# Optimization experiments

Hardware: AMD Instinct MI355X
Metric: run time of the kernel (lower is better)

The kernel has to match this reference:

```python
import jax, jax.numpy as jnp
import numpy as np
from jax import lax


def setup_inputs() -> dict:
    key = jax.random.key(0)
    k1, k2 = jax.random.split(key)
    X = jax.random.normal(k1, (32, 64, 112, 112), dtype=jnp.float32)
    # module draws K ~ N(0, 0.01) each forward; we materialize it as a param
    K = 0.01 * jax.random.normal(k2, (128, 64, 3, 3), dtype=jnp.float32)
    return {"X": X, "K": K}


def reference(X, K):
    # Valid-padding cross-correlation, NCHW input, OIHW kernel, no bias.
    # Matches conv2d_multi_out: sum over in_channels, stack over out_channels.
    return lax.conv_general_dilated(
        X, K,
        window_strides=(1, 1),
        padding="VALID",
        dimension_numbers=("NCHW", "OIHW", "NCHW"),
    )
```

## Files before the change

kernel.cpp:

```cpp
#include <hip/hip_runtime.h>


typedef __attribute__((ext_vector_type(8)))  _Float16 f16x8;
typedef __attribute__((ext_vector_type(16))) float    f32x16;

struct __attribute__((aligned(4))) f2u { float x, y; };

constexpr int C_IN = 64, H = 112, W = 112;
constexpr int COUT = 128, OH = 110, OW = 110;
constexpr int NIMG = 32;
constexpr int KTOT = C_IN * 9;
constexpr int OSP  = OH * OW;
constexpr int SPTOT = NIMG * OSP;
constexpr int IMG_STRIDE = C_IN * H * W;
constexpr int CH_STRIDE  = H * W;
constexpr int LDC = 72;

__device__ __forceinline__ uint pkrtz_u32(float lo, float hi) {
    union { __fp16 __attribute__((ext_vector_type(2))) h; uint u; } c;
    c.h = __builtin_amdgcn_cvt_pkrtz(lo, hi);
    return c.u;
}

__device__ __forceinline__ int swz(int row, int chw) {
    return row * LDC + (chw ^ (((row >> 1) & 7) << 3));
}

__global__ void prep_a(const float* __restrict__ Kw, _Float16* __restrict__ A16) {
    int idx = blockIdx.x * 256 + threadIdx.x;
    if (idx >= COUT * KTOT) return;
    int cout = idx / KTOT, k = idx - cout * KTOT;
    int c = k / 9, s = k - c * 9;
    int o = c >> 3, j = c & 7;
    A16[((size_t)(s * 8 + o) * COUT + cout) * 8 + j] = (_Float16)Kw[idx];
}

__global__ __launch_bounds__(512, 4)
void conv_shift_f16(const float* __restrict__ X,
                    const _Float16* __restrict__ A16,
                    float* __restrict__ Out)
{
    __shared__ __align__(16) _Float16 Bs[2][128 * LDC];

    const int t = threadIdx.x;

    const int nwg = gridDim.x;
    const int q8 = nwg >> 3, r8 = nwg & 7;
    const int xcd = blockIdx.x & 7, idx8 = blockIdx.x >> 3;
    const int bid = (xcd < r8 ? xcd * (q8 + 1) : r8 * (q8 + 1) + (xcd - r8) * q8) + idx8;
    const int spBase = bid * 128;

    const int spp = t & 63;
    const int c0  = (t >> 6) << 3;
    const int sp0 = spBase + 2 * spp;
    const int nimg = sp0 / OSP;
    const int rsp  = sp0 - nimg * OSP;
    const int oh   = rsp / OW;
    const int ow   = rsp - oh * OW;
    const float* Xr = X + ((size_t)nimg * IMG_STRIDE + (size_t)c0 * CH_STRIDE + oh * W + ow);
    const int whw0 = swz(2 * spp,     c0);
    const int whw1 = swz(2 * spp + 1, c0);

    const int lane  = t & 63;
    const int wv    = t >> 6;
    const int wq    = wv >> 1;
    const int wc    = wv & 1;
    const int frow  = lane & 31;
    const int khalf = lane >> 5;
    const size_t arow = (size_t)(wq * 32 + frow) * 8;
    const int bmask = ((frow >> 1) & 7) << 3;
    const int brw0  = (wc * 64 + frow) * LDC;
    const int brw1  = (wc * 64 + 32 + frow) * LDC;

    f32x16 acc[2];
#pragma unroll
    for (int j = 0; j < 2; j++)
#pragma unroll
        for (int e = 0; e < 16; e++) acc[j][e] = 0.f;

    f2u g[8];

#define SOFF(S) (((S) / 3) * W + ((S) % 3))

#define GATHER(S)                                                              \
    {                                                                          \
        _Pragma("unroll")                                                      \
        for (int j = 0; j < 8; j++)                                            \
            g[j] = *reinterpret_cast<const f2u*>(Xr + (size_t)j * CH_STRIDE + SOFF(S)); \
    }

#define CVTWRITE(BUF)                                                          \
    {                                                                          \
        union { uint u[4]; f16x8 v; } px, py;                                  \
        _Pragma("unroll")                                                      \
        for (int p = 0; p < 4; p++) {                                          \
            px.u[p] = pkrtz_u32(g[2 * p].x, g[2 * p + 1].x);                   \
            py.u[p] = pkrtz_u32(g[2 * p].y, g[2 * p + 1].y);                   \
        }                                                                      \
        *reinterpret_cast<f16x8*>(&Bs[BUF][whw0]) = px.v;                      \
        *reinterpret_cast<f16x8*>(&Bs[BUF][whw1]) = py.v;                      \
    }

#define MFMA_STEP(S, B)                                                        \
    {                                                                          \
        _Pragma("unroll")                                                      \
        for (int kk = 0; kk < 4; kk++) {                                       \
            const size_t abase = (size_t)((S) * 8 + kk * 2 + khalf) * (COUT * 8) + arow; \
            const int chw = (kk * 16 + khalf * 8) ^ bmask;                     \
            f16x8 a0 = *reinterpret_cast<const f16x8*>(&A16[abase]);           \
            f16x8 b0 = *reinterpret_cast<const f16x8*>(&Bs[B][brw0 + chw]);    \
            f16x8 b1 = *reinterpret_cast<const f16x8*>(&Bs[B][brw1 + chw]);    \
            acc[0] = __builtin_amdgcn_mfma_f32_32x32x16_f16(a0, b0, acc[0], 0, 0, 0); \
            acc[1] = __builtin_amdgcn_mfma_f32_32x32x16_f16(a0, b1, acc[1], 0, 0, 0); \
        }                                                                      \
    }

    GATHER(0);
    CVTWRITE(0);
    GATHER(1);
    __syncthreads();

#pragma unroll
    for (int s = 0; s < 9; s++) {
        if (s < 8) CVTWRITE((s + 1) & 1);
        if (s < 7) GATHER(s + 2);
        MFMA_STEP(s, s & 1);
        __syncthreads();
    }

#undef GATHER
#undef CVTWRITE
#undef MFMA_STEP
#undef SOFF

#pragma unroll
    for (int j = 0; j < 2; j++) {
        const int sp2 = spBase + wc * 64 + j * 32 + frow;
        const int n2  = sp2 / OSP;
        const int r2  = sp2 - n2 * OSP;
        float* Ob = Out + (size_t)n2 * (COUT * OSP) + r2;
        const int cbase = wq * 32 + 4 * khalf;
#pragma unroll
        for (int reg = 0; reg < 16; reg++) {
            const int crow = cbase + (reg & 3) + 8 * (reg >> 2);
            Ob[(size_t)crow * OSP] = acc[j][reg];
        }
    }
}

extern "C" void kernel_launch(void* const* d_in, const int* in_sizes, int n_in,
                              void* d_out, int out_size, void* d_ws, size_t ws_size,
                              hipStream_t stream) {
    const float* X  = (const float*)d_in[0];
    const float* Kw = (const float*)d_in[1];
    float* Out = (float*)d_out;
    _Float16* A16 = (_Float16*)d_ws;

    prep_a<<<(COUT * KTOT + 255) / 256, 256, 0, stream>>>(Kw, A16);
    conv_shift_f16<<<SPTOT / 128, 512, 0, stream>>>(X, A16, Out);
}
```

Measured before the change: 111.6 us.

## Stage input rows in LDS once and reuse across all nine filter taps

Each workgroup now handles two output rows of one image. It loads the four input rows it needs, for all 64 channels, into shared memory as fp16 with a channel-slot swizzle. All 3x3 taps then read shifted windows of that staged tile instead of re-gathering X from global memory for every tap. This removes the 9x redundant global gather and the per-tap double buffering and barriers. In exchange, LDS use is larger (about 57KB), which may limit occupancy. About 220 of 256 spatial columns are used, so some MFMA work is wasted on padding.

Result: slower. 123.2 us (+10.5%).

```diff
diff --git a/kernel.cpp b/kernel.cpp
--- a/kernel.cpp
+++ b/kernel.cpp
@@ -4,26 +4,21 @@
 typedef __attribute__((ext_vector_type(8)))  _Float16 f16x8;
 typedef __attribute__((ext_vector_type(16))) float    f32x16;
 
-struct __attribute__((aligned(4))) f2u { float x, y; };
-
 constexpr int C_IN = 64, H = 112, W = 112;
 constexpr int COUT = 128, OH = 110, OW = 110;
 constexpr int NIMG = 32;
 constexpr int KTOT = C_IN * 9;
 constexpr int OSP  = OH * OW;
-constexpr int SPTOT = NIMG * OSP;
 constexpr int IMG_STRIDE = C_IN * H * W;
 constexpr int CH_STRIDE  = H * W;
-constexpr int LDC = 72;
+constexpr int ROWS = 4;
+constexpr int NRP  = OH / 2;
+constexpr int NWG  = NIMG * NRP;
 
 __device__ __forceinline__ uint pkrtz_u32(float lo, float hi) {
     union { __fp16 __attribute__((ext_vector_type(2))) h; uint u; } c;
     c.h = __builtin_amdgcn_cvt_pkrtz(lo, hi);
     return c.u;
-}
-
-__device__ __forceinline__ int swz(int row, int chw) {
-    return row * LDC + (chw ^ (((row >> 1) & 7) << 3));
 }
 
 __global__ void prep_a(const float* __restrict__ Kw, _Float16* __restrict__ A16) {
@@ -36,114 +31,105 @@
 }
 
 __global__ __launch_bounds__(512, 4)
-void conv_shift_f16(const float* __restrict__ X,
-                    const _Float16* __restrict__ A16,
-                    float* __restrict__ Out)
+void conv_resx_f16(const float* __restrict__ X,
+                   const _Float16* __restrict__ A16,
+                   float* __restrict__ Out)
 {
-    __shared__ __align__(16) _Float16 Bs[2][128 * LDC];
+    __shared__ __align__(16) _Float16 Xs[ROWS * W * C_IN];
 
     const int t = threadIdx.x;
 
-    const int nwg = gridDim.x;
-    const int q8 = nwg >> 3, r8 = nwg & 7;
-    const int xcd = blockIdx.x & 7, idx8 = blockIdx.x >> 3;
-    const int bid = (xcd < r8 ? xcd * (q8 + 1) : r8 * (q8 + 1) + (xcd - r8) * q8) + idx8;
-    const int spBase = bid * 128;
+    const int bid = (blockIdx.x & 7) * (NWG >> 3) + (blockIdx.x >> 3);
+    const int n   = bid / NRP;
+    const int rp  = bid - n * NRP;
+    const int oh0 = rp * 2;
 
-    const int spp = t & 63;
-    const int c0  = (t >> 6) << 3;
-    const int sp0 = spBase + 2 * spp;
-    const int nimg = sp0 / OSP;
-    const int rsp  = sp0 - nimg * OSP;
-    const int oh   = rsp / OW;
-    const int ow   = rsp - oh * OW;
-    const float* Xr = X + ((size_t)nimg * IMG_STRIDE + (size_t)c0 * CH_STRIDE + oh * W + ow);
-    const int whw0 = swz(2 * spp,     c0);
-    const int whw1 = swz(2 * spp + 1, c0);
+    const float* Xn = X + (size_t)n * IMG_STRIDE + (size_t)oh0 * W;
+
+    if (t < 448) {
+#pragma unroll
+        for (int q = 0; q < 4; q++) {
+            const int tau = q * 448 + t;
+            const int cg  = tau / 224;
+            const int wpr = tau - cg * 224;
+            const int row = wpr / 56;
+            const int wcl = (wpr - row * 56) * 2;
+            const float* src = Xn + (size_t)(cg * 8) * CH_STRIDE + row * W + wcl;
+            float2 v[8];
+#pragma unroll
+            for (int j = 0; j < 8; j++)
+                v[j] = *reinterpret_cast<const float2*>(src + (size_t)j * CH_STRIDE);
+            union { uint u[4]; f16x8 h; } p0, p1;
+#pragma unroll
+            for (int p = 0; p < 4; p++) {
+                p0.u[p] = pkrtz_u32(v[2 * p].x, v[2 * p + 1].x);
+                p1.u[p] = pkrtz_u32(v[2 * p].y, v[2 * p + 1].y);
+            }
+            const int a0 = (row * W + wcl)     * C_IN + ((cg ^ (wcl & 7)) << 3);
+            const int a1 = (row * W + wcl + 1) * C_IN + ((cg ^ ((wcl + 1) & 7)) << 3);
+            *reinterpret_cast<f16x8*>(&Xs[a0]) = p0.h;
+            *reinterpret_cast<f16x8*>(&Xs[a1]) = p1.h;
+        }
+    }
 
     const int lane  = t & 63;
     const int wv    = t >> 6;
-    const int wq    = wv >> 1;
-    const int wc    = wv & 1;
+    const int cq    = wv & 3;
+    const int sh    = wv >> 2;
     const int frow  = lane & 31;
     const int khalf = lane >> 5;
-    const size_t arow = (size_t)(wq * 32 + frow) * 8;
-    const int bmask = ((frow >> 1) & 7) << 3;
-    const int brw0  = (wc * 64 + frow) * LDC;
-    const int brw1  = (wc * 64 + 32 + frow) * LDC;
 
-    f32x16 acc[2];
+    int bbase[4], owv[4];
 #pragma unroll
-    for (int j = 0; j < 2; j++)
-#pragma unroll
-        for (int e = 0; e < 16; e++) acc[j][e] = 0.f;
-
-    f2u g[8];
-
-#define SOFF(S) (((S) / 3) * W + ((S) % 3))
-
-#define GATHER(S)                                                              \
-    {                                                                          \
-        _Pragma("unroll")                                                      \
-        for (int j = 0; j < 8; j++)                                            \
-            g[j] = *reinterpret_cast<const f2u*>(Xr + (size_t)j * CH_STRIDE + SOFF(S)); \
+    for (int i = 0; i < 4; i++) {
+        int spl = (sh * 4 + i) * 32 + frow;
+        int s2  = (spl < 220) ? spl : 0;
+        int orow = (s2 >= 110) ? 1 : 0;
+        int ow   = s2 - orow * 110;
+        bbase[i] = (orow * W + ow) * C_IN;
+        owv[i]   = ow;
     }
 
-#define CVTWRITE(BUF)                                                          \
-    {                                                                          \
-        union { uint u[4]; f16x8 v; } px, py;                                  \
-        _Pragma("unroll")                                                      \
-        for (int p = 0; p < 4; p++) {                                          \
-            px.u[p] = pkrtz_u32(g[2 * p].x, g[2 * p + 1].x);                   \
-            py.u[p] = pkrtz_u32(g[2 * p].y, g[2 * p + 1].y);                   \
-        }                                                                      \
-        *reinterpret_cast<f16x8*>(&Bs[BUF][whw0]) = px.v;                      \
-        *reinterpret_cast<f16x8*>(&Bs[BUF][whw1]) = py.v;                      \
-    }
+    f32x16 acc[4];
+#pragma unroll
+    for (int i = 0; i < 4; i++)
+#pragma unroll
+        for (int e = 0; e < 16; e++) acc[i][e] = 0.f;
 
-#define MFMA_STEP(S, B)                                                        \
-    {                                                                          \
-        _Pragma("unroll")                                                      \
-        for (int kk = 0; kk < 4; kk++) {                                       \
-            const size_t abase = (size_t)((S) * 8 + kk * 2 + khalf) * (COUT * 8) + arow; \
-            const int chw = (kk * 16 + khalf * 8) ^ bmask;                     \
-            f16x8 a0 = *reinterpret_cast<const f16x8*>(&A16[abase]);           \
-            f16x8 b0 = *reinterpret_cast<const f16x8*>(&Bs[B][brw0 + chw]);    \
-            f16x8 b1 = *reinterpret_cast<const f16x8*>(&Bs[B][brw1 + chw]);    \
-            acc[0] = __builtin_amdgcn_mfma_f32_32x32x16_f16(a0, b0, acc[0], 0, 0, 0); \
-            acc[1] = __builtin_amdgcn_mfma_f32_32x32x16_f16(a0, b1, acc[1], 0, 0, 0); \
-        }                                                                      \
-    }
-
-    GATHER(0);
-    CVTWRITE(0);
-    GATHER(1);
     __syncthreads();
 
 #pragma unroll
     for (int s = 0; s < 9; s++) {
-        if (s < 8) CVTWRITE((s + 1) & 1);
-        if (s < 7) GATHER(s + 2);
-        MFMA_STEP(s, s & 1);
-        __syncthreads();
+        const int kh = s / 3, kw = s % 3;
+        const int soff = (kh * W + kw) * C_IN;
+#pragma unroll
+        for (int kk = 0; kk < 4; kk++) {
+            const int oct = kk * 2;
+            const f16x8 a = *reinterpret_cast<const f16x8*>(
+                &A16[((size_t)((s * 8 + oct + khalf) * COUT) + cq * 32 + frow) * 8]);
+#pragma unroll
+            for (int i = 0; i < 4; i++) {
+                const int slot = ((oct + khalf) ^ ((owv[i] + kw) & 7)) << 3;
+                const f16x8 b = *reinterpret_cast<const f16x8*>(
+                    &Xs[bbase[i] + soff + slot]);
+                acc[i] = __builtin_amdgcn_mfma_f32_32x32x16_f16(a, b, acc[i], 0, 0, 0);
+            }
+        }
     }
 
-#undef GATHER
-#undef CVTWRITE
-#undef MFMA_STEP
-#undef SOFF
-
+    float* On = Out + (size_t)n * (COUT * (size_t)OSP) + (size_t)(cq * 32 + 4 * khalf) * OSP;
 #pragma unroll
-    for (int j = 0; j < 2; j++) {
-        const int sp2 = spBase + wc * 64 + j * 32 + frow;
-        const int n2  = sp2 / OSP;
-        const int r2  = sp2 - n2 * OSP;
-        float* Ob = Out + (size_t)n2 * (COUT * OSP) + r2;
-        const int cbase = wq * 32 + 4 * khalf;
+    for (int i = 0; i < 4; i++) {
+        const int spl = (sh * 4 + i) * 32 + frow;
+        if (spl < 220) {
+            const int orow = (spl >= 110) ? 1 : 0;
+            const int ow   = spl - orow * 110;
+            float* Ob = On + (size_t)(oh0 + orow) * OW + ow;
 #pragma unroll
-        for (int reg = 0; reg < 16; reg++) {
-            const int crow = cbase + (reg & 3) + 8 * (reg >> 2);
-            Ob[(size_t)crow * OSP] = acc[j][reg];
+            for (int reg = 0; reg < 16; reg++) {
+                const int crow = (reg & 3) + 8 * (reg >> 2);
+                Ob[(size_t)crow * OSP] = acc[i][reg];
+            }
         }
     }
 }
@@ -157,5 +143,5 @@
     _Float16* A16 = (_Float16*)d_ws;
 
     prep_a<<<(COUT * KTOT + 255) / 256, 256, 0, stream>>>(Kw, A16);
-    conv_shift_f16<<<SPTOT / 128, 512, 0, stream>>>(X, A16, Out);
+    conv_resx_f16<<<NWG, 512, 0, stream>>>(X, A16, Out);
 }
```

## Halve block size, stage weights in LDS via async loads, widen per-wave tile

Applied to the files above, without the earlier changes.

Moves from 512 to 256 threads per block, with each wave now computing 32 output channels across all 128 spatial positions (four accumulators instead of two). Weight slices for each filter tap are copied into a double-buffered LDS area with global_load_lds, so each A fragment is loaded once per step and reused across four MFMAs. Each thread now gathers 16 input channels per tap instead of 8, and the LDS swizzle is rewritten to match. This trades more registers and LDS per block, plus lower occupancy, for fewer global weight reads and more MFMA work per LDS read.

Result: slower. 141.8 us (+27.0%).

```diff
diff --git a/kernel.cpp b/kernel.cpp
--- a/kernel.cpp
+++ b/kernel.cpp
@@ -15,6 +15,7 @@
 constexpr int IMG_STRIDE = C_IN * H * W;
 constexpr int CH_STRIDE  = H * W;
 constexpr int LDC = 72;
+constexpr int ASLICE = 8 * COUT * 8;
 
 __device__ __forceinline__ uint pkrtz_u32(float lo, float hi) {
     union { __fp16 __attribute__((ext_vector_type(2))) h; uint u; } c;
@@ -22,9 +23,8 @@
     return c.u;
 }
 
-__device__ __forceinline__ int swz(int row, int chw) {
-    return row * LDC + (chw ^ (((row >> 1) & 7) << 3));
-}
+typedef __attribute__((address_space(3))) uint       lds_u32;
+typedef __attribute__((address_space(1))) const uint glb_u32;
 
 __global__ void prep_a(const float* __restrict__ Kw, _Float16* __restrict__ A16) {
     int idx = blockIdx.x * 256 + threadIdx.x;
@@ -35,12 +35,13 @@
     A16[((size_t)(s * 8 + o) * COUT + cout) * 8 + j] = (_Float16)Kw[idx];
 }
 
-__global__ __launch_bounds__(512, 4)
-void conv_shift_f16(const float* __restrict__ X,
-                    const _Float16* __restrict__ A16,
-                    float* __restrict__ Out)
+__global__ __launch_bounds__(256, 2)
+void conv_v6(const float* __restrict__ X,
+             const _Float16* __restrict__ A16,
+             float* __restrict__ Out)
 {
     __shared__ __align__(16) _Float16 Bs[2][128 * LDC];
+    __shared__ __align__(16) _Float16 As[2][ASLICE];
 
     const int t = threadIdx.x;
 
@@ -51,95 +52,115 @@
     const int spBase = bid * 128;
 
     const int spp = t & 63;
-    const int c0  = (t >> 6) << 3;
+    const int chh = t >> 6;
     const int sp0 = spBase + 2 * spp;
     const int nimg = sp0 / OSP;
     const int rsp  = sp0 - nimg * OSP;
     const int oh   = rsp / OW;
     const int ow   = rsp - oh * OW;
-    const float* Xr = X + ((size_t)nimg * IMG_STRIDE + (size_t)c0 * CH_STRIDE + oh * W + ow);
-    const int whw0 = swz(2 * spp,     c0);
-    const int whw1 = swz(2 * spp + 1, c0);
+    const float* Xb = X + ((size_t)nimg * IMG_STRIDE + (size_t)(chh * 16) * CH_STRIDE + oh * W + ow);
+    const int gsw = spp & 7;
+    const int wr0 = (2 * spp) * LDC;
+    const int wr1 = (2 * spp + 1) * LDC;
 
     const int lane  = t & 63;
-    const int wv    = t >> 6;
-    const int wq    = wv >> 1;
-    const int wc    = wv & 1;
+    const int cq    = t >> 6;
     const int frow  = lane & 31;
     const int khalf = lane >> 5;
-    const size_t arow = (size_t)(wq * 32 + frow) * 8;
-    const int bmask = ((frow >> 1) & 7) << 3;
-    const int brw0  = (wc * 64 + frow) * LDC;
-    const int brw1  = (wc * 64 + 32 + frow) * LDC;
+    const int bsw   = ((frow >> 1) & 7);
 
-    f32x16 acc[2];
+    f32x16 acc[4];
 #pragma unroll
-    for (int j = 0; j < 2; j++)
+    for (int j = 0; j < 4; j++)
 #pragma unroll
         for (int e = 0; e < 16; e++) acc[j][e] = 0.f;
 
-    f2u g[8];
+    f2u g[16];
 
 #define SOFF(S) (((S) / 3) * W + ((S) % 3))
 
 #define GATHER(S)                                                              \
     {                                                                          \
         _Pragma("unroll")                                                      \
-        for (int j = 0; j < 8; j++)                                            \
-            g[j] = *reinterpret_cast<const f2u*>(Xr + (size_t)j * CH_STRIDE + SOFF(S)); \
+        for (int c = 0; c < 16; c++)                                           \
+            g[c] = *reinterpret_cast<const f2u*>(Xb + (size_t)c * CH_STRIDE + SOFF(S)); \
     }
 
-#define CVTWRITE(BUF)                                                          \
+#define CVTWRITE(B)                                                            \
     {                                                                          \
-        union { uint u[4]; f16x8 v; } px, py;                                  \
         _Pragma("unroll")                                                      \
-        for (int p = 0; p < 4; p++) {                                          \
-            px.u[p] = pkrtz_u32(g[2 * p].x, g[2 * p + 1].x);                   \
-            py.u[p] = pkrtz_u32(g[2 * p].y, g[2 * p + 1].y);                   \
+        for (int o = 0; o < 2; o++) {                                          \
+            union { uint u[4]; f16x8 v; } px, py;                              \
+            _Pragma("unroll")                                                  \
+            for (int p = 0; p < 4; p++) {                                      \
+                px.u[p] = pkrtz_u32(g[o * 8 + 2 * p].x, g[o * 8 + 2 * p + 1].x); \
+                py.u[p] = pkrtz_u32(g[o * 8 + 2 * p].y, g[o * 8 + 2 * p + 1].y); \
+            }                                                                  \
+            const int slot = ((chh * 2 + o) ^ gsw) << 3;                       \
+            *reinterpret_cast<f16x8*>(&Bs[B][wr0 + slot]) = px.v;              \
+            *reinterpret_cast<f16x8*>(&Bs[B][wr1 + slot]) = py.v;              \
         }                                                                      \
-        *reinterpret_cast<f16x8*>(&Bs[BUF][whw0]) = px.v;                      \
-        *reinterpret_cast<f16x8*>(&Bs[BUF][whw1]) = py.v;                      \
     }
 
-#define MFMA_STEP(S, B)                                                        \
+#define ACOPY(S, B)                                                            \
+    {                                                                          \
+        const _Float16* gsrc = A16 + (size_t)(S)*ASLICE;                       \
+        _Pragma("unroll")                                                      \
+        for (int q = 0; q < 4; q++) {                                          \
+            const int unit = (cq * 4 + q) * 64 + lane;                         \
+            __builtin_amdgcn_global_load_lds(                                  \
+                (glb_u32*)(gsrc + unit * 8),                                   \
+                (lds_u32*)(&As[B][unit * 8]), 16, 0, 0);                       \
+        }                                                                      \
+    }
+
+#define MFMA_STEP(B)                                                           \
     {                                                                          \
         _Pragma("unroll")                                                      \
         for (int kk = 0; kk < 4; kk++) {                                       \
-            const size_t abase = (size_t)((S) * 8 + kk * 2 + khalf) * (COUT * 8) + arow; \
-            const int chw = (kk * 16 + khalf * 8) ^ bmask;                     \
-            f16x8 a0 = *reinterpret_cast<const f16x8*>(&A16[abase]);           \
-            f16x8 b0 = *reinterpret_cast<const f16x8*>(&Bs[B][brw0 + chw]);    \
-            f16x8 b1 = *reinterpret_cast<const f16x8*>(&Bs[B][brw1 + chw]);    \
-            acc[0] = __builtin_amdgcn_mfma_f32_32x32x16_f16(a0, b0, acc[0], 0, 0, 0); \
-            acc[1] = __builtin_amdgcn_mfma_f32_32x32x16_f16(a0, b1, acc[1], 0, 0, 0); \
+            const int oct = kk * 2 + khalf;                                    \
+            const f16x8 a = *reinterpret_cast<const f16x8*>(                   \
+                &As[B][(oct * COUT + cq * 32 + frow) * 8]);                    \
+            _Pragma("unroll")                                                  \
+            for (int j = 0; j < 4; j++) {                                      \
+                const int slot = (oct ^ bsw) << 3;                             \
+                const f16x8 b = *reinterpret_cast<const f16x8*>(               \
+                    &Bs[B][(j * 32 + frow) * LDC + slot]);                     \
+                acc[j] = __builtin_amdgcn_mfma_f32_32x32x16_f16(a, b, acc[j], 0, 0, 0); \
+            }                                                                  \
         }                                                                      \
     }
 
     GATHER(0);
+    ACOPY(0, 0);
     CVTWRITE(0);
     GATHER(1);
     __syncthreads();
 
 #pragma unroll
     for (int s = 0; s < 9; s++) {
-        if (s < 8) CVTWRITE((s + 1) & 1);
+        if (s < 8) {
+            ACOPY(s + 1, (s + 1) & 1);
+            CVTWRITE((s + 1) & 1);
+        }
         if (s < 7) GATHER(s + 2);
-        MFMA_STEP(s, s & 1);
+        MFMA_STEP(s & 1);
         __syncthreads();
     }
 
 #undef GATHER
 #undef CVTWRITE
+#undef ACOPY
 #undef MFMA_STEP
 #undef SOFF
 
+    const int cbase = cq * 32 + 4 * khalf;
 #pragma unroll
-    for (int j = 0; j < 2; j++) {
-        const int sp2 = spBase + wc * 64 + j * 32 + frow;
+    for (int j = 0; j < 4; j++) {
+        const int sp2 = spBase + j * 32 + frow;
         const int n2  = sp2 / OSP;
         const int r2  = sp2 - n2 * OSP;
-        float* Ob = Out + (size_t)n2 * (COUT * OSP) + r2;
-        const int cbase = wq * 32 + 4 * khalf;
+        float* Ob = Out + (size_t)n2 * (COUT * (size_t)OSP) + r2;
 #pragma unroll
         for (int reg = 0; reg < 16; reg++) {
             const int crow = cbase + (reg & 3) + 8 * (reg >> 2);
@@ -157,5 +178,5 @@
     _Float16* A16 = (_Float16*)d_ws;
 
     prep_a<<<(COUT * KTOT + 255) / 256, 256, 0, stream>>>(Kw, A16);
-    conv_shift_f16<<<SPTOT / 128, 512, 0, stream>>>(X, A16, Out);
+    conv_v6<<<SPTOT / 128, 256, 0, stream>>>(X, A16, Out);
 }
```
